# Kernel tuning notes

Measured on AMD Instinct MI355X. Metric: run time of the kernel, lower is better.

The kernel has to match this reference:

```python
import jax, jax.numpy as jnp
import numpy as np

N_NODES = 100000
N_EDGES = 1600000
DIM = 128


def setup_inputs() -> dict:
    key = jax.random.key(0)
    k_x, k_e, k_wm, k_bm, k_wu, k_bu = jax.random.split(key, 6)
    bound = 1.0 / np.sqrt(DIM)
    return {
        "x": jax.random.normal(k_x, (N_NODES, DIM), dtype=jnp.float32),
        "edge_index": jax.random.randint(k_e, (2, N_EDGES), 0, N_NODES, dtype=jnp.int64),
        "W_msg": jax.random.uniform(k_wm, (DIM, DIM), jnp.float32, -bound, bound),
        "b_msg": jax.random.uniform(k_bm, (DIM,), jnp.float32, -bound, bound),
        "W_upd": jax.random.uniform(k_wu, (DIM, DIM), jnp.float32, -bound, bound),
        "b_upd": jax.random.uniform(k_bu, (DIM,), jnp.float32, -bound, bound),
    }


def reference(x, edge_index, W_msg, b_msg, W_upd, b_upd):
    # message_net: Linear + ReLU on all nodes  [N, D]
    messages = jax.nn.relu(x @ W_msg.T + b_msg)
    src, dst = edge_index[0], edge_index[1]
    # gather by src, scatter-add by dst (index_add)  [N, D]
    aggregated = jax.ops.segment_sum(messages[src], dst, num_segments=x.shape[0])
    # update_net: Linear + ReLU, then residual
    updated = jax.nn.relu(aggregated @ W_upd.T + b_upd)
    return updated + x
```

## Files before the change

### kernel.cpp

```cpp
#include <hip/hip_runtime.h>
#include <hip/hip_bf16.h>

#define DIM 128
#define BNODES 128
#define NBMAX 1024
#define BCAP 4096

typedef __attribute__((ext_vector_type(8))) short bf16x8;
typedef __attribute__((ext_vector_type(4))) float f32x4;

__device__ inline ushort f2bf(float f) {
    uint u = __float_as_uint(f);
    u += 0x7fffu + ((u >> 16) & 1u);
    return (ushort)(u >> 16);
}
__device__ inline uint pack2(float lo, float hi) {
    return (uint)f2bf(lo) | ((uint)f2bf(hi) << 16);
}

template<bool RESID, bool BF16OUT>
__global__ __launch_bounds__(256, 2)
void linear_mfma_kernel(const float* in, const float* __restrict__ W,
                        const float* __restrict__ b, const float* __restrict__ xres,
                        void* outv, int n_tiles)
{
    __shared__ uint4 Wl[128 * 16];

    const int t = threadIdx.x;
    for (int q = t; q < 2048; q += 256) {
        const int j = q >> 4, c = q & 15;
        const float4 lo = ((const float4*)(W + j * 128 + c * 8))[0];
        const float4 hi = ((const float4*)(W + j * 128 + c * 8))[1];
        uint4 pk;
        pk.x = pack2(lo.x, lo.y); pk.y = pack2(lo.z, lo.w);
        pk.z = pack2(hi.x, hi.y); pk.w = pack2(hi.z, hi.w);
        Wl[j * 16 + (c ^ (j & 15))] = pk;
    }
    __syncthreads();

    const int lane = t & 63;
    const int lo4 = lane & 15;
    const int g   = lane >> 4;

    float bias[8];
    #pragma unroll
    for (int ct = 0; ct < 8; ++ct) bias[ct] = b[ct * 16 + lo4];

    const int wid = (blockIdx.x * 256 + t) >> 6;
    const int nw  = (gridDim.x * 256) >> 6;

    for (int tile = wid; tile < n_tiles; tile += nw) {
        const int arow = tile * 16 + lo4;
        const float4* ap = (const float4*)(in + (size_t)arow * DIM + g * 32);
        float4 v[8];
        #pragma unroll
        for (int i = 0; i < 8; ++i) v[i] = ap[i];

        bf16x8 afrag[4];
        #pragma unroll
        for (int ks = 0; ks < 4; ++ks) {
            union { bf16x8 v8; uint u[4]; } a;
            a.u[0] = pack2(v[2*ks].x,   v[2*ks].y);
            a.u[1] = pack2(v[2*ks].z,   v[2*ks].w);
            a.u[2] = pack2(v[2*ks+1].x, v[2*ks+1].y);
            a.u[3] = pack2(v[2*ks+1].z, v[2*ks+1].w);
            afrag[ks] = a.v8;
        }

        f32x4 acc[8];
        #pragma unroll
        for (int ct = 0; ct < 8; ++ct)
            acc[ct] = (f32x4){bias[ct], bias[ct], bias[ct], bias[ct]};

        #pragma unroll
        for (int ks = 0; ks < 4; ++ks) {
            #pragma unroll
            for (int ct = 0; ct < 8; ++ct) {
                const int jrow = ct * 16 + lo4;
                const bf16x8 bfrag = *((const bf16x8*)&Wl[jrow * 16 + ((g * 4 + ks) ^ lo4)]);
                acc[ct] = __builtin_amdgcn_mfma_f32_16x16x32_bf16(afrag[ks], bfrag, acc[ct], 0, 0, 0);
            }
        }

        #pragma unroll
        for (int ct = 0; ct < 8; ++ct) {
            #pragma unroll
            for (int r = 0; r < 4; ++r) {
                const int orow = tile * 16 + g * 4 + r;
                const int ocol = ct * 16 + lo4;
                float val = fmaxf(acc[ct][r], 0.f);
                if constexpr (RESID) val += xres[(size_t)orow * DIM + ocol];
                if constexpr (BF16OUT)
                    ((ushort*)outv)[(size_t)orow * DIM + ocol] = f2bf(val);
                else
                    ((float*)outv)[(size_t)orow * DIM + ocol] = val;
            }
        }
    }
}

__global__ __launch_bounds__(256)
void bucket_scatter_kernel(const int* __restrict__ ei, int* __restrict__ gcur,
                           uint* __restrict__ bedges, int n_edges, int nb)
{
    __shared__ int histL[NBMAX];
    __shared__ int curL[NBMAX];
    const int t = threadIdx.x;
    for (int i = t; i < nb; i += 256) histL[i] = 0;
    __syncthreads();
    const int chunk = (n_edges + gridDim.x - 1) / gridDim.x;
    const int e0 = blockIdx.x * chunk;
    const int e1 = min(e0 + chunk, n_edges);
    for (int e = e0 + t; e < e1; e += 256)
        atomicAdd(&histL[ei[n_edges + e] >> 7], 1);
    __syncthreads();
    for (int i = t; i < nb; i += 256)
        curL[i] = histL[i] ? atomicAdd(&gcur[i], histL[i]) : 0;
    __syncthreads();
    for (int e = e0 + t; e < e1; e += 256) {
        const int src = ei[e];
        const int dst = ei[n_edges + e];
        const int b = dst >> 7;
        const int pos = atomicAdd(&curL[b], 1);
        if (pos < BCAP)
            bedges[(size_t)b * BCAP + pos] = ((uint)src << 7) | (uint)(dst & 127);
    }
}

__global__ __launch_bounds__(512)
void bucket_gather_kernel(const uint* __restrict__ msg, const int* __restrict__ gcur,
                          const uint* __restrict__ bedges, float* __restrict__ agg,
                          int n_nodes)
{
    __shared__ uint edgesL[BCAP];
    __shared__ int  srcL[BCAP];
    __shared__ int histL[BNODES];
    __shared__ int inclL[BNODES];
    __shared__ int cursL[BNODES];

    const int t = threadIdx.x;
    const int b = blockIdx.x;
    const int cnt = min(gcur[b], BCAP);
    const uint* be = bedges + (size_t)b * BCAP;

    if (t < BNODES) histL[t] = 0;
    __syncthreads();
    for (int i = t; i < cnt; i += 512) {
        const uint p = be[i];
        edgesL[i] = p;
        atomicAdd(&histL[p & 127u], 1);
    }
    __syncthreads();
    if (t < BNODES) inclL[t] = histL[t];
    for (int off = 1; off < BNODES; off <<= 1) {
        int add = 0;
        __syncthreads();
        if (t < BNODES && t >= off) add = inclL[t - off];
        __syncthreads();
        if (t < BNODES) inclL[t] += add;
    }
    __syncthreads();
    if (t < BNODES) cursL[t] = inclL[t] - histL[t];
    __syncthreads();
    for (int i = t; i < cnt; i += 512) {
        const uint p = edgesL[i];
        const int pos = atomicAdd(&cursL[p & 127u], 1);
        srcL[pos] = (int)(p >> 7);
    }
    __syncthreads();

    const int lane = t & 63;
    const int w = t >> 6;
    for (int dl = w; dl < BNODES; dl += 8) {
        const int node = b * BNODES + dl;
        if (node >= n_nodes) break;
        const int e1 = inclL[dl];
        const int e0 = e1 - histL[dl];
        float a0 = 0.f, a1 = 0.f;
        int i = e0;
        for (; i + 4 <= e1; i += 4) {
            const int sA = srcL[i + 0], sB = srcL[i + 1];
            const int sC = srcL[i + 2], sD = srcL[i + 3];
            const uint mA = msg[(size_t)sA * 64 + lane];
            const uint mB = msg[(size_t)sB * 64 + lane];
            const uint mC = msg[(size_t)sC * 64 + lane];
            const uint mD = msg[(size_t)sD * 64 + lane];
            a0 += __uint_as_float(mA << 16) + __uint_as_float(mB << 16)
                + __uint_as_float(mC << 16) + __uint_as_float(mD << 16);
            a1 += __uint_as_float(mA & 0xffff0000u) + __uint_as_float(mB & 0xffff0000u)
                + __uint_as_float(mC & 0xffff0000u) + __uint_as_float(mD & 0xffff0000u);
        }
        for (; i < e1; ++i) {
            const uint m = msg[(size_t)srcL[i] * 64 + lane];
            a0 += __uint_as_float(m << 16);
            a1 += __uint_as_float(m & 0xffff0000u);
        }
        ((float2*)(agg + (size_t)node * DIM))[lane] = make_float2(a0, a1);
    }
}

extern "C" void kernel_launch(void* const* d_in, const int* in_sizes, int n_in,
                              void* d_out, int out_size, void* d_ws, size_t ws_size,
                              hipStream_t stream)
{
    const float* x  = (const float*)d_in[0];
    const int*   ei = (const int*)d_in[1];
    const float* Wm = (const float*)d_in[2];
    const float* bm = (const float*)d_in[3];
    const float* Wu = (const float*)d_in[4];
    const float* bu = (const float*)d_in[5];

    const int N = in_sizes[0] / DIM;
    const int E = in_sizes[1] / 2;
    const int nb = (N + BNODES - 1) / BNODES;

    char* ws = (char*)d_ws;
    ushort* msg = (ushort*)ws;
    size_t o = (size_t)N * DIM * sizeof(ushort);
    int* gcur = (int*)(ws + o); o += (size_t)NBMAX * 4;
    o = (o + 255) & ~(size_t)255;
    uint* bedges = (uint*)(ws + o);

    float* out = (float*)d_out;
    float* agg = out;

    const int n_tiles = N / 16;

    linear_mfma_kernel<false, true><<<1024, 256, 0, stream>>>(x, Wm, bm, nullptr, msg, n_tiles);

    hipMemsetAsync(gcur, 0, (size_t)nb * 4, stream);
    bucket_scatter_kernel<<<1024, 256, 0, stream>>>(ei, gcur, bedges, E, nb);

    bucket_gather_kernel<<<nb, 512, 0, stream>>>((const uint*)msg, gcur, bedges, agg, N);

    linear_mfma_kernel<true, false><<<1024, 256, 0, stream>>>(agg, Wu, bu, x, out, n_tiles);
}
```

Baseline: 165.5 us.

## Split edge bucketing into coarse and fine two-pass scatter

Replaces the single-pass scatter of edges into 782 fine buckets with a two-level radix-style scatter. The first pass sorts edges into about 98 coarse buckets of 1024 nodes, and the second pass splits each coarse bucket into 8 fine buckets. The goal is fewer scattered write destinations per block, giving better write coalescing and less global atomic contention. The cost is an extra kernel launch and an extra read and write of all edges through a new intermediate buffer.

```diff
diff --git a/kernel.cpp b/kernel.cpp
--- a/kernel.cpp
+++ b/kernel.cpp
@@ -3,8 +3,12 @@
 
 #define DIM 128
 #define BNODES 128
+#define CNODES 1024
+#define NCMAX 128
 #define NBMAX 1024
+#define CCAP 20480
 #define BCAP 4096
+#define SPLITB 8
 
 typedef __attribute__((ext_vector_type(8))) short bf16x8;
 typedef __attribute__((ext_vector_type(4))) float f32x4;
@@ -100,30 +104,62 @@
 }
 
 __global__ __launch_bounds__(256)
-void bucket_scatter_kernel(const int* __restrict__ ei, int* __restrict__ gcur,
-                           uint* __restrict__ bedges, int n_edges, int nb)
-{
-    __shared__ int histL[NBMAX];
-    __shared__ int curL[NBMAX];
-    const int t = threadIdx.x;
-    for (int i = t; i < nb; i += 256) histL[i] = 0;
+void coarse_scatter_kernel(const int* __restrict__ ei, int* __restrict__ ccur,
+                           uint* __restrict__ cedges, int n_edges, int ncb)
+{
+    __shared__ int histL[NCMAX];
+    __shared__ int curL[NCMAX];
+    const int t = threadIdx.x;
+    if (t < ncb) histL[t] = 0;
     __syncthreads();
     const int chunk = (n_edges + gridDim.x - 1) / gridDim.x;
     const int e0 = blockIdx.x * chunk;
     const int e1 = min(e0 + chunk, n_edges);
     for (int e = e0 + t; e < e1; e += 256)
-        atomicAdd(&histL[ei[n_edges + e] >> 7], 1);
-    __syncthreads();
-    for (int i = t; i < nb; i += 256)
-        curL[i] = histL[i] ? atomicAdd(&gcur[i], histL[i]) : 0;
+        atomicAdd(&histL[ei[n_edges + e] >> 10], 1);
+    __syncthreads();
+    if (t < ncb)
+        curL[t] = histL[t] ? atomicAdd(&ccur[t], histL[t]) : 0;
     __syncthreads();
     for (int e = e0 + t; e < e1; e += 256) {
         const int src = ei[e];
         const int dst = ei[n_edges + e];
-        const int b = dst >> 7;
-        const int pos = atomicAdd(&curL[b], 1);
+        const int c = dst >> 10;
+        const int pos = atomicAdd(&curL[c], 1);
+        if (pos < CCAP)
+            cedges[(size_t)c * CCAP + pos] = ((uint)src << 10) | (uint)(dst & 1023);
+    }
+}
+
+__global__ __launch_bounds__(256)
+void fine_scatter_kernel(const int* __restrict__ ccnt, const uint* __restrict__ cedges,
+                         int* __restrict__ gcur, uint* __restrict__ bedges, int ncb)
+{
+    __shared__ int histL[SPLITB];
+    __shared__ int curL[SPLITB];
+    const int t = threadIdx.x;
+    const int c = blockIdx.x / SPLITB;
+    const int s = blockIdx.x % SPLITB;
+    const int cnt = min(ccnt[c], CCAP);
+    const int chunk = (cnt + SPLITB - 1) / SPLITB;
+    const int e0 = s * chunk;
+    const int e1 = min(e0 + chunk, cnt);
+    if (t < SPLITB) histL[t] = 0;
+    __syncthreads();
+    const uint* ce = cedges + (size_t)c * CCAP;
+    for (int i = e0 + t; i < e1; i += 256)
+        atomicAdd(&histL[(ce[i] & 1023u) >> 7], 1);
+    __syncthreads();
+    if (t < SPLITB)
+        curL[t] = histL[t] ? atomicAdd(&gcur[c * SPLITB + t], histL[t]) : 0;
+    __syncthreads();
+    for (int i = e0 + t; i < e1; i += 256) {
+        const uint p = ce[i];
+        const uint dl = p & 1023u;
+        const int f = (int)(dl >> 7);
+        const int pos = atomicAdd(&curL[f], 1);
         if (pos < BCAP)
-            bedges[(size_t)b * BCAP + pos] = ((uint)src << 7) | (uint)(dst & 127);
+            bedges[(size_t)(c * SPLITB + f) * BCAP + pos] = ((p >> 10) << 7) | (dl & 127u);
     }
 }
 
@@ -212,13 +248,17 @@
 
     const int N = in_sizes[0] / DIM;
     const int E = in_sizes[1] / 2;
-    const int nb = (N + BNODES - 1) / BNODES;
+    const int nb  = (N + BNODES - 1) / BNODES;
+    const int ncb = (N + CNODES - 1) / CNODES;
 
     char* ws = (char*)d_ws;
     ushort* msg = (ushort*)ws;
     size_t o = (size_t)N * DIM * sizeof(ushort);
+    int* ccur = (int*)(ws + o); o += (size_t)NCMAX * 4;
     int* gcur = (int*)(ws + o); o += (size_t)NBMAX * 4;
     o = (o + 255) & ~(size_t)255;
+    uint* cedges = (uint*)(ws + o); o += (size_t)ncb * CCAP * 4;
+    o = (o + 255) & ~(size_t)255;
     uint* bedges = (uint*)(ws + o);
 
     float* out = (float*)d_out;
@@ -228,8 +268,9 @@
 
     linear_mfma_kernel<false, true><<<1024, 256, 0, stream>>>(x, Wm, bm, nullptr, msg, n_tiles);
 
-    hipMemsetAsync(gcur, 0, (size_t)nb * 4, stream);
-    bucket_scatter_kernel<<<1024, 256, 0, stream>>>(ei, gcur, bedges, E, nb);
+    hipMemsetAsync(ccur, 0, (size_t)(NCMAX + NBMAX) * 4, stream);
+    coarse_scatter_kernel<<<1024, 256, 0, stream>>>(ei, ccur, cedges, E, ncb);
+    fine_scatter_kernel<<<ncb * SPLITB, 256, 0, stream>>>(ccur, cedges, gcur, bedges, ncb);
 
     bucket_gather_kernel<<<nb, 512, 0, stream>>>((const uint*)msg, gcur, bedges, agg, N);
 
```

Measured after the change: 157.6 us. -4.7%, faster.
